# Kernel optimization log

Hardware: AMD Instinct MI355X
Metric: run time of the kernel (lower is better)

Reference implementation:

```python
import jax, jax.numpy as jnp
import numpy as np

TEMP = 0.07
POS_WINDOW = 2
EPS = 1e-8
NEG = -1e9  # finite large-negative for masking (safe under vjp)


def _l2norm(x):
    # matches F.normalize(dim=-1) with eps=1e-12
    n = jnp.sqrt(jnp.sum(x * x, axis=-1, keepdims=True))
    return x / jnp.maximum(n, 1e-12)


def setup_inputs() -> dict:
    key = jax.random.key(0)
    k1, k2, k3, k4, k5 = jax.random.split(key, 5)
    B, T, D = 32, 1024, 256
    eeg_enc = jax.random.normal(k1, (B, T, D), dtype=jnp.float32)
    eye_enc = jax.random.normal(k2, (B, T, D), dtype=jnp.float32)
    mask = jax.random.randint(k3, (B, T), 0, 2, dtype=jnp.int32)
    W_eeg = jax.random.normal(k4, (D, D), dtype=jnp.float32) / np.sqrt(D)
    W_eye = jax.random.normal(k5, (D, D), dtype=jnp.float32) / np.sqrt(D)
    return {"eeg_enc": eeg_enc, "eye_enc": eye_enc, "mask": mask,
            "W_eeg": W_eeg, "W_eye": W_eye}


def reference(eeg_enc, eye_enc, mask, W_eeg, W_eye):
    B, T, D = eeg_enc.shape
    valid = mask > 0  # (B,T)
    # nn.Linear(bias=False): x @ W.T, then L2-normalize
    e = _l2norm(jnp.einsum('btd,ed->bte', eeg_enc, W_eeg))
    v = _l2norm(jnp.einsum('btd,ed->bte', eye_enc, W_eye))
    sims = jnp.einsum('bid,bjd->bij', e, v) / TEMP  # (B,T,T)
    # rank of each valid step within the compressed (gathered) ordering
    rank = jnp.cumsum(valid.astype(jnp.int32), axis=-1) - 1  # (B,T)
    band = jnp.abs(rank[:, :, None] - rank[:, None, :]) <= POS_WINDOW
    pair = valid[:, :, None] & valid[:, None, :]  # both steps valid
    pos = pair & band
    # per-row max over positive (banded) entries
    pos_scores = jnp.max(jnp.where(pos, sims, NEG), axis=-1)  # (B,T)
    # logsumexp over valid columns (the gathered sims row)
    lse = jax.nn.logsumexp(jnp.where(valid[:, None, :], sims, NEG), axis=-1)
    row_loss = -(pos_scores - lse)  # (B,T)
    Tv = jnp.sum(valid, axis=-1)  # (B,)
    per_b = jnp.sum(jnp.where(valid, row_loss, 0.0), axis=-1) / jnp.maximum(Tv, 1)
    per_b = jnp.where(Tv >= 2, per_b, 0.0)  # skip samples with <2 valid steps
    return jnp.sum(per_b) / (B + EPS)
```

## Files before the change

kernel.cpp:

```cpp
#include <hip/hip_runtime.h>
#include <hip/hip_bf16.h>

typedef __attribute__((ext_vector_type(8))) short bf16x8;
typedef __attribute__((ext_vector_type(4))) float f32x4;

#define INVT (1.0f/0.07f)

static __device__ __forceinline__ short f2bf(float f){
    unsigned int u = __float_as_uint(f);
    unsigned int r = (u + 0x7fffu + ((u >> 16) & 1u)) >> 16;
    return (short)r;
}
static __device__ __forceinline__ float bf2f(short s){
    return __uint_as_float(((unsigned int)(unsigned short)s) << 16);
}

static __device__ __forceinline__ void gld16(const void* g, void* l){
    __builtin_amdgcn_global_load_lds(
        (const __attribute__((address_space(1))) unsigned int*)g,
        (__attribute__((address_space(3))) unsigned int*)l, 16, 0, 0);
}

__global__ __launch_bounds__(256) void prep_kernel(const float* __restrict__ Weeg,
                                                   const float* __restrict__ Weye,
                                                   const int* __restrict__ mask,
                                                   short* __restrict__ Wout,
                                                   int* __restrict__ rank,
                                                   int* __restrict__ idx,
                                                   int* __restrict__ Tv,
                                                   float* __restrict__ cb,
                                                   float* __restrict__ bsum){
    __shared__ int ssum[256];
    int tid = threadIdx.x;
    if (blockIdx.x < 512){
        int i = blockIdx.x * 256 + tid;
        float v = (i < 65536) ? Weeg[i] : Weye[i - 65536];
        Wout[i] = f2bf(v);
        return;
    }
    int b = blockIdx.x - 512;
    if (tid == 0) bsum[b] = 0.f;
    int local[4]; int s = 0;
    #pragma unroll
    for (int q = 0; q < 4; ++q){
        int t = tid*4 + q;
        local[q] = (mask[b*1024 + t] > 0) ? 1 : 0;
        s += local[q];
    }
    ssum[tid] = s;
    __syncthreads();
    for (int off = 1; off < 256; off <<= 1){
        int add = (tid >= off) ? ssum[tid - off] : 0;
        __syncthreads();
        ssum[tid] += add;
        __syncthreads();
    }
    int run = ssum[tid] - s;
    #pragma unroll
    for (int q = 0; q < 4; ++q){
        int t = tid*4 + q;
        int g = b*1024 + t;
        run += local[q];
        rank[g] = run - 1;
        cb[g]   = local[q] ? 0.0f : -1e9f;
        if (local[q]) idx[b*1024 + run - 1] = t;
    }
    if (tid == 255) Tv[b] = ssum[255];
}

__global__ __launch_bounds__(256, 2) void proj_kernel(const float* __restrict__ Aeeg,
                                                      const float* __restrict__ Aeye,
                                                      const short* __restrict__ Wbf,
                                                      short* __restrict__ Eout,
                                                      short* __restrict__ Vout){
    __shared__ short sW[2][64 * 256];
    int sel = blockIdx.y;
    const float* A   = sel ? Aeye : Aeeg;
    const short* W   = Wbf + sel * 65536;
    short*       Out = sel ? Vout : Eout;

    int tid = threadIdx.x;
    int w = tid >> 6, lane = tid & 63;
    int l15 = lane & 15, lq = lane >> 4;
    int kb  = lq * 8;
    int row0 = blockIdx.x * 64;

    int ro   = lane >> 5;
    int cs   = lane & 31;
    int s7   = l15 & 7;

    #pragma unroll
    for (int p = 0; p < 8; ++p){
        int rr = (p*2 + ro) & 7;
        gld16(W + (size_t)(w*16 + p*2 + ro)*256 + (cs ^ rr)*8,
              &sW[0][(w*16 + p*2) * 256]);
    }
    #pragma unroll
    for (int p = 0; p < 8; ++p){
        int rr = (p*2 + ro) & 7;
        gld16(W + (size_t)(64 + w*16 + p*2 + ro)*256 + (cs ^ rr)*8,
              &sW[1][(w*16 + p*2) * 256]);
    }

    bf16x8 xf[8];
    {
        const float* ap = A + (size_t)(row0 + w*16 + l15) * 256 + kb;
        #pragma unroll
        for (int g = 0; g < 8; ++g){
            float4 x0 = *(const float4*)(ap + g*32);
            float4 x1 = *(const float4*)(ap + g*32 + 4);
            bf16x8 t;
            t[0]=f2bf(x0.x); t[1]=f2bf(x0.y); t[2]=f2bf(x0.z); t[3]=f2bf(x0.w);
            t[4]=f2bf(x1.x); t[5]=f2bf(x1.y); t[6]=f2bf(x1.z); t[7]=f2bf(x1.w);
            xf[g] = t;
        }
    }

    f32x4 acc[16];
    #pragma unroll
    for (int q = 0; q < 16; ++q) acc[q] = (f32x4){0.f,0.f,0.f,0.f};

    __syncthreads();

    #pragma unroll
    for (int nt = 0; nt < 4; ++nt){
        f32x4 c = acc[nt];
        int rbase = (nt*16 + l15) * 256;
        #pragma unroll
        for (int g = 0; g < 8; ++g){
            bf16x8 wf = *(const bf16x8*)&sW[0][rbase + (((g*4 + lq) ^ s7) << 3)];
            c = __builtin_amdgcn_mfma_f32_16x16x32_bf16(wf, xf[g], c, 0, 0, 0);
        }
        acc[nt] = c;
    }

    __syncthreads();

    #pragma unroll
    for (int p = 0; p < 8; ++p){
        int rr = (p*2 + ro) & 7;
        gld16(W + (size_t)(128 + w*16 + p*2 + ro)*256 + (cs ^ rr)*8,
              &sW[0][(w*16 + p*2) * 256]);
    }
    #pragma unroll
    for (int nt = 0; nt < 4; ++nt){
        f32x4 c = acc[4 + nt];
        int rbase = (nt*16 + l15) * 256;
        #pragma unroll
        for (int g = 0; g < 8; ++g){
            bf16x8 wf = *(const bf16x8*)&sW[1][rbase + (((g*4 + lq) ^ s7) << 3)];
            c = __builtin_amdgcn_mfma_f32_16x16x32_bf16(wf, xf[g], c, 0, 0, 0);
        }
        acc[4 + nt] = c;
    }

    __syncthreads();

    #pragma unroll
    for (int p = 0; p < 8; ++p){
        int rr = (p*2 + ro) & 7;
        gld16(W + (size_t)(192 + w*16 + p*2 + ro)*256 + (cs ^ rr)*8,
              &sW[1][(w*16 + p*2) * 256]);
    }
    #pragma unroll
    for (int nt = 0; nt < 4; ++nt){
        f32x4 c = acc[8 + nt];
        int rbase = (nt*16 + l15) * 256;
        #pragma unroll
        for (int g = 0; g < 8; ++g){
            bf16x8 wf = *(const bf16x8*)&sW[0][rbase + (((g*4 + lq) ^ s7) << 3)];
            c = __builtin_amdgcn_mfma_f32_16x16x32_bf16(wf, xf[g], c, 0, 0, 0);
        }
        acc[8 + nt] = c;
    }

    __syncthreads();

    #pragma unroll
    for (int nt = 0; nt < 4; ++nt){
        f32x4 c = acc[12 + nt];
        int rbase = (nt*16 + l15) * 256;
        #pragma unroll
        for (int g = 0; g < 8; ++g){
            bf16x8 wf = *(const bf16x8*)&sW[1][rbase + (((g*4 + lq) ^ s7) << 3)];
            c = __builtin_amdgcn_mfma_f32_16x16x32_bf16(wf, xf[g], c, 0, 0, 0);
        }
        acc[12 + nt] = c;
    }

    float ss = 0.f;
    #pragma unroll
    for (int q = 0; q < 16; ++q){
        #pragma unroll
        for (int r = 0; r < 4; ++r){ float x = acc[q][r]; ss += x*x; }
    }
    ss += __shfl_xor(ss, 16);
    ss += __shfl_xor(ss, 32);
    float scale = 1.0f / fmaxf(sqrtf(ss), 1e-12f);

    short* twrow = &sW[0][(w*16 + l15) * 256];
    #pragma unroll
    for (int q = 0; q < 16; ++q){
        short4 pk;
        pk.x = f2bf(acc[q][0] * scale);
        pk.y = f2bf(acc[q][1] * scale);
        pk.z = f2bf(acc[q][2] * scale);
        pk.w = f2bf(acc[q][3] * scale);
        int c    = (q >> 2) * 64 + (q & 3) * 16 + lq*4;
        int blk  = (c >> 3) ^ s7;
        *(short4*)(twrow + blk*8 + (c & 7)) = pk;
    }
    short* op = Out + (size_t)(row0 + w*16) * 256;
    #pragma unroll
    for (int p = 0; p < 8; ++p){
        int rloc = p*2 + (lane >> 5);
        int gblk = lane & 31;
        const short* tr = &sW[0][(w*16 + rloc) * 256 + ((gblk ^ (rloc & 7)) * 8)];
        *(int4*)(op + rloc*256 + gblk*8) = *(const int4*)tr;
    }
}

__global__ __launch_bounds__(64) void loss_kernel(const short* __restrict__ E,
                                                  const short* __restrict__ V,
                                                  const float* __restrict__ cb,
                                                  float* __restrict__ psum){
    int n  = blockIdx.x;
    int b  = (((n >> 3) & 3) << 3) | (n & 7);
    int r2 = n >> 5;
    int it = r2 & 15;
    int jq = r2 >> 4;

    int lane = threadIdx.x;
    int l15 = lane & 15, lq = lane >> 4;

    bf16x8 af[4][8];
    {
        const short* ep = E + ((size_t)b*1024 + it*64 + l15) * 256 + lq*8;
        #pragma unroll
        for (int s = 0; s < 4; ++s)
            #pragma unroll
            for (int g = 0; g < 8; ++g)
                af[s][g] = *(const bf16x8*)(ep + s*16*256 + g*32);
    }

    const short* vp  = V  + ((size_t)b*1024 + jq*256 + l15) * 256 + lq*8;
    const float* cbp = cb + b*1024 + jq*256 + l15;

    float ls[4][4];
    #pragma unroll
    for (int s = 0; s < 4; ++s)
        #pragma unroll
        for (int r = 0; r < 4; ++r) ls[s][r] = 0.f;

    bf16x8 ba[8], bb[8];
    #pragma unroll
    for (int g = 0; g < 8; ++g) ba[g] = *(const bf16x8*)(vp + g*32);
    float ca = cbp[0];
    float cbv;

    #pragma unroll 1
    for (int t = 0; t < 8; ++t){
        {
            const short* v1 = vp + (size_t)(2*t + 1) * 16 * 256;
            #pragma unroll
            for (int g = 0; g < 8; ++g) bb[g] = *(const bf16x8*)(v1 + g*32);
            cbv = cbp[(2*t + 1) * 16];
        }
        {
            f32x4 a0 = (f32x4){0.f,0.f,0.f,0.f};
            f32x4 a1 = (f32x4){0.f,0.f,0.f,0.f};
            f32x4 a2 = (f32x4){0.f,0.f,0.f,0.f};
            f32x4 a3 = (f32x4){0.f,0.f,0.f,0.f};
            #pragma unroll
            for (int g = 0; g < 8; ++g){
                a0 = __builtin_amdgcn_mfma_f32_16x16x32_bf16(af[0][g], ba[g], a0, 0, 0, 0);
                a1 = __builtin_amdgcn_mfma_f32_16x16x32_bf16(af[1][g], ba[g], a1, 0, 0, 0);
                a2 = __builtin_amdgcn_mfma_f32_16x16x32_bf16(af[2][g], ba[g], a2, 0, 0, 0);
                a3 = __builtin_amdgcn_mfma_f32_16x16x32_bf16(af[3][g], ba[g], a3, 0, 0, 0);
            }
            #pragma unroll
            for (int r = 0; r < 4; ++r){
                ls[0][r] += __expf(fmaf(a0[r], INVT, ca));
                ls[1][r] += __expf(fmaf(a1[r], INVT, ca));
                ls[2][r] += __expf(fmaf(a2[r], INVT, ca));
                ls[3][r] += __expf(fmaf(a3[r], INVT, ca));
            }
        }
        if (t < 7){
            const short* v2 = vp + (size_t)(2*t + 2) * 16 * 256;
            #pragma unroll
            for (int g = 0; g < 8; ++g) ba[g] = *(const bf16x8*)(v2 + g*32);
            ca = cbp[(2*t + 2) * 16];
        }
        {
            f32x4 a0 = (f32x4){0.f,0.f,0.f,0.f};
            f32x4 a1 = (f32x4){0.f,0.f,0.f,0.f};
            f32x4 a2 = (f32x4){0.f,0.f,0.f,0.f};
            f32x4 a3 = (f32x4){0.f,0.f,0.f,0.f};
            #pragma unroll
            for (int g = 0; g < 8; ++g){
                a0 = __builtin_amdgcn_mfma_f32_16x16x32_bf16(af[0][g], bb[g], a0, 0, 0, 0);
                a1 = __builtin_amdgcn_mfma_f32_16x16x32_bf16(af[1][g], bb[g], a1, 0, 0, 0);
                a2 = __builtin_amdgcn_mfma_f32_16x16x32_bf16(af[2][g], bb[g], a2, 0, 0, 0);
                a3 = __builtin_amdgcn_mfma_f32_16x16x32_bf16(af[3][g], bb[g], a3, 0, 0, 0);
            }
            #pragma unroll
            for (int r = 0; r < 4; ++r){
                ls[0][r] += __expf(fmaf(a0[r], INVT, cbv));
                ls[1][r] += __expf(fmaf(a1[r], INVT, cbv));
                ls[2][r] += __expf(fmaf(a2[r], INVT, cbv));
                ls[3][r] += __expf(fmaf(a3[r], INVT, cbv));
            }
        }
    }

    #pragma unroll
    for (int s = 0; s < 4; ++s)
        #pragma unroll
        for (int r = 0; r < 4; ++r){
            float v = ls[s][r];
            #pragma unroll
            for (int mm = 1; mm < 16; mm <<= 1)
                v += __shfl_xor(v, mm);
            ls[s][r] = v;
        }

    if (l15 == 0){
        float* pp = psum + (size_t)jq*32768 + (size_t)b*1024 + it*64;
        #pragma unroll
        for (int s = 0; s < 4; ++s)
            #pragma unroll
            for (int r = 0; r < 4; ++r)
                pp[s*16 + lq*4 + r] = ls[s][r];
    }
}

__global__ __launch_bounds__(256) void pos_kernel(const short* __restrict__ E,
                                                  const short* __restrict__ V,
                                                  const int* __restrict__ mask,
                                                  const int* __restrict__ rank,
                                                  const int* __restrict__ idx,
                                                  const int* __restrict__ Tv,
                                                  float* __restrict__ pmax){
    int tid = threadIdx.x;
    int gl  = tid & 15;
    int rf  = (blockIdx.x * 256 + tid) >> 4;
    int b   = rf >> 10;
    if (mask[rf] <= 0) return;

    int ri = rank[rf];
    int tv = Tv[b];
    int lo = ri - 2; if (lo < 0) lo = 0;
    int hi = ri + 2; if (hi > tv - 1) hi = tv - 1;

    const short* epp = E + (size_t)rf * 256 + gl * 16;
    float ev[16];
    {
        bf16x8 e0 = *(const bf16x8*)epp;
        bf16x8 e1 = *(const bf16x8*)(epp + 8);
        #pragma unroll
        for (int k = 0; k < 8; ++k){ ev[k] = bf2f(e0[k]); ev[8+k] = bf2f(e1[k]); }
    }
    float pm = -1e30f;
    for (int r = lo; r <= hi; ++r){
        int j = idx[b*1024 + r];
        const short* vpp = V + ((size_t)(b*1024) + j) * 256 + gl * 16;
        bf16x8 v0 = *(const bf16x8*)vpp;
        bf16x8 v1 = *(const bf16x8*)(vpp + 8);
        float s = 0.f;
        #pragma unroll
        for (int k = 0; k < 8; ++k){
            s = fmaf(ev[k],   bf2f(v0[k]), s);
            s = fmaf(ev[8+k], bf2f(v1[k]), s);
        }
        s += __shfl_xor(s, 1);
        s += __shfl_xor(s, 2);
        s += __shfl_xor(s, 4);
        s += __shfl_xor(s, 8);
        pm = fmaxf(pm, s);
    }
    if (gl == 0) pmax[rf] = pm * INVT;
}

__global__ __launch_bounds__(256) void reduce_kernel(const float* __restrict__ psum,
                                                     const float* __restrict__ pmax,
                                                     const int* __restrict__ mask,
                                                     float* __restrict__ bsum){
    int b  = blockIdx.x >> 2;
    int i  = (blockIdx.x & 3) * 256 + threadIdx.x;
    int g  = b*1024 + i;
    float a = 0.f;
    if (mask[g] > 0){
        float ps = psum[g] + psum[g + 32768] + psum[g + 65536] + psum[g + 98304];
        a = logf(ps) - pmax[g];
    }
    #pragma unroll
    for (int m = 1; m < 64; m <<= 1) a += __shfl_xor(a, m);
    if ((threadIdx.x & 63) == 0 && a != 0.f) atomicAdd(&bsum[b], a);
}

__global__ void final_kernel(const float* __restrict__ bsum,
                             const int* __restrict__ Tv,
                             float* __restrict__ out){
    int tid = threadIdx.x;
    float v = 0.f;
    if (tid < 32){
        int tv = Tv[tid];
        if (tv >= 2) v = bsum[tid] / (float)tv;
    }
    #pragma unroll
    for (int m = 1; m < 64; m <<= 1) v += __shfl_xor(v, m);
    if (tid == 0) out[0] = v / 32.0f;
}

extern "C" void kernel_launch(void* const* d_in, const int* in_sizes, int n_in,
                              void* d_out, int out_size, void* d_ws, size_t ws_size,
                              hipStream_t stream) {
    const float* eeg  = (const float*)d_in[0];
    const float* eye  = (const float*)d_in[1];
    const int*   mask = (const int*)d_in[2];
    const float* Weeg = (const float*)d_in[3];
    const float* Weye = (const float*)d_in[4];
    float* out = (float*)d_out;

    char* ws = (char*)d_ws;
    short* e_bf  = (short*)(ws);
    short* v_bf  = (short*)(ws + 16777216);
    short* wbf   = (short*)(ws + 33554432);
    int*   rank  = (int*)  (ws + 33816576);
    int*   idx   = (int*)  (ws + 33947648);
    float* cb    = (float*)(ws + 34078720);
    float* psum  = (float*)(ws + 34209792);
    float* pmax  = (float*)(ws + 34734080);
    int*   Tv    = (int*)  (ws + 34865152);
    float* bsum  = (float*)(ws + 34865280);

    prep_kernel<<<544, 256, 0, stream>>>(Weeg, Weye, mask, wbf, rank, idx, Tv, cb, bsum);
    proj_kernel<<<dim3(512, 2), 256, 0, stream>>>(eeg, eye, wbf, e_bf, v_bf);
    loss_kernel<<<2048, 64, 0, stream>>>(e_bf, v_bf, cb, psum);
    pos_kernel<<<2048, 256, 0, stream>>>(e_bf, v_bf, mask, rank, idx, Tv, pmax);
    reduce_kernel<<<128, 256, 0, stream>>>(psum, pmax, mask, bsum);
    final_kernel<<<1, 64, 0, stream>>>(bsum, Tv, out);
}
```

Baseline: 172.6 us.

## Share V tiles across four waves via double-buffered LDS in loss kernel

Reworks the loss kernel from 64-thread blocks that each load their own V rows from global memory into 256-thread blocks. In these blocks four waves share 16-row V tiles, staged into a swizzled, double-buffered LDS buffer with async global-to-LDS loads. This cuts redundant global/L2 traffic for V by four times and frees the B-operand registers. It adds block-wide barriers each half-iteration and LDS read traffic, and reduces the grid from 2048 to 512 blocks, which may lower latency hiding.

```diff
diff --git a/kernel.cpp b/kernel.cpp
--- a/kernel.cpp
+++ b/kernel.cpp
@@ -220,22 +220,39 @@
     }
 }
 
-__global__ __launch_bounds__(64) void loss_kernel(const short* __restrict__ E,
-                                                  const short* __restrict__ V,
-                                                  const float* __restrict__ cb,
-                                                  float* __restrict__ psum){
-    int n  = blockIdx.x;
-    int b  = (((n >> 3) & 3) << 3) | (n & 7);
-    int r2 = n >> 5;
-    int it = r2 & 15;
-    int jq = r2 >> 4;
-
-    int lane = threadIdx.x;
-    int l15 = lane & 15, lq = lane >> 4;
+__global__ __launch_bounds__(256, 2) void loss_kernel(const short* __restrict__ E,
+                                                      const short* __restrict__ V,
+                                                      const float* __restrict__ cb,
+                                                      float* __restrict__ psum){
+    __shared__ short sV[2][16 * 256];
+
+    int n   = blockIdx.x;
+    int b   = (((n >> 3) & 3) << 3) | (n & 7);
+    int itg = (n >> 5) & 3;
+    int jq  = n >> 7;
+
+    int tid  = threadIdx.x;
+    int w    = tid >> 6, lane = tid & 63;
+    int l15  = lane & 15, lq = lane >> 4;
+    int s7   = l15 & 7;
+    int ro   = lane >> 5;
+    int cs   = lane & 31;
+    int j0   = jq * 256;
+    int i0   = itg * 256 + w * 64;
+
+    const short* Vb = V + (size_t)b * 1024 * 256;
+
+    #pragma unroll
+    for (int c0 = 0; c0 < 2; ++c0){
+        int p  = w*2 + c0;
+        int rr = (p*2 + ro) & 7;
+        gld16(Vb + (size_t)(j0 + p*2 + ro)*256 + (cs ^ rr)*8,
+              &sV[0][(p*2) * 256]);
+    }
 
     bf16x8 af[4][8];
     {
-        const short* ep = E + ((size_t)b*1024 + it*64 + l15) * 256 + lq*8;
+        const short* ep = E + ((size_t)b*1024 + i0 + l15) * 256 + lq*8;
         #pragma unroll
         for (int s = 0; s < 4; ++s)
             #pragma unroll
@@ -243,8 +260,7 @@
                 af[s][g] = *(const bf16x8*)(ep + s*16*256 + g*32);
     }
 
-    const short* vp  = V  + ((size_t)b*1024 + jq*256 + l15) * 256 + lq*8;
-    const float* cbp = cb + b*1024 + jq*256 + l15;
+    const float* cbp = cb + b*1024 + j0 + l15;
 
     float ls[4][4];
     #pragma unroll
@@ -252,31 +268,30 @@
         #pragma unroll
         for (int r = 0; r < 4; ++r) ls[s][r] = 0.f;
 
-    bf16x8 ba[8], bb[8];
-    #pragma unroll
-    for (int g = 0; g < 8; ++g) ba[g] = *(const bf16x8*)(vp + g*32);
-    float ca = cbp[0];
-    float cbv;
+    __syncthreads();
 
     #pragma unroll 1
-    for (int t = 0; t < 8; ++t){
+    for (int tp = 0; tp < 8; ++tp){
+        #pragma unroll
+        for (int c0 = 0; c0 < 2; ++c0){
+            int p  = w*2 + c0;
+            int rr = (p*2 + ro) & 7;
+            gld16(Vb + (size_t)(j0 + (2*tp+1)*16 + p*2 + ro)*256 + (cs ^ rr)*8,
+                  &sV[1][(p*2) * 256]);
+        }
         {
-            const short* v1 = vp + (size_t)(2*t + 1) * 16 * 256;
-            #pragma unroll
-            for (int g = 0; g < 8; ++g) bb[g] = *(const bf16x8*)(v1 + g*32);
-            cbv = cbp[(2*t + 1) * 16];
-        }
-        {
+            float ca = cbp[2*tp*16];
             f32x4 a0 = (f32x4){0.f,0.f,0.f,0.f};
             f32x4 a1 = (f32x4){0.f,0.f,0.f,0.f};
             f32x4 a2 = (f32x4){0.f,0.f,0.f,0.f};
             f32x4 a3 = (f32x4){0.f,0.f,0.f,0.f};
             #pragma unroll
             for (int g = 0; g < 8; ++g){
-                a0 = __builtin_amdgcn_mfma_f32_16x16x32_bf16(af[0][g], ba[g], a0, 0, 0, 0);
-                a1 = __builtin_amdgcn_mfma_f32_16x16x32_bf16(af[1][g], ba[g], a1, 0, 0, 0);
-                a2 = __builtin_amdgcn_mfma_f32_16x16x32_bf16(af[2][g], ba[g], a2, 0, 0, 0);
-                a3 = __builtin_amdgcn_mfma_f32_16x16x32_bf16(af[3][g], ba[g], a3, 0, 0, 0);
+                bf16x8 bf = *(const bf16x8*)&sV[0][l15*256 + (((g*4 + lq) ^ s7) << 3)];
+                a0 = __builtin_amdgcn_mfma_f32_16x16x32_bf16(af[0][g], bf, a0, 0, 0, 0);
+                a1 = __builtin_amdgcn_mfma_f32_16x16x32_bf16(af[1][g], bf, a1, 0, 0, 0);
+                a2 = __builtin_amdgcn_mfma_f32_16x16x32_bf16(af[2][g], bf, a2, 0, 0, 0);
+                a3 = __builtin_amdgcn_mfma_f32_16x16x32_bf16(af[3][g], bf, a3, 0, 0, 0);
             }
             #pragma unroll
             for (int r = 0; r < 4; ++r){
@@ -286,32 +301,40 @@
                 ls[3][r] += __expf(fmaf(a3[r], INVT, ca));
             }
         }
-        if (t < 7){
-            const short* v2 = vp + (size_t)(2*t + 2) * 16 * 256;
-            #pragma unroll
-            for (int g = 0; g < 8; ++g) ba[g] = *(const bf16x8*)(v2 + g*32);
-            ca = cbp[(2*t + 2) * 16];
+        __syncthreads();
+
+        if (tp < 7){
+            #pragma unroll
+            for (int c0 = 0; c0 < 2; ++c0){
+                int p  = w*2 + c0;
+                int rr = (p*2 + ro) & 7;
+                gld16(Vb + (size_t)(j0 + (2*tp+2)*16 + p*2 + ro)*256 + (cs ^ rr)*8,
+                      &sV[0][(p*2) * 256]);
+            }
         }
         {
+            float ca = cbp[(2*tp+1)*16];
             f32x4 a0 = (f32x4){0.f,0.f,0.f,0.f};
             f32x4 a1 = (f32x4){0.f,0.f,0.f,0.f};
             f32x4 a2 = (f32x4){0.f,0.f,0.f,0.f};
             f32x4 a3 = (f32x4){0.f,0.f,0.f,0.f};
             #pragma unroll
             for (int g = 0; g < 8; ++g){
-                a0 = __builtin_amdgcn_mfma_f32_16x16x32_bf16(af[0][g], bb[g], a0, 0, 0, 0);
-                a1 = __builtin_amdgcn_mfma_f32_16x16x32_bf16(af[1][g], bb[g], a1, 0, 0, 0);
-                a2 = __builtin_amdgcn_mfma_f32_16x16x32_bf16(af[2][g], bb[g], a2, 0, 0, 0);
-                a3 = __builtin_amdgcn_mfma_f32_16x16x32_bf16(af[3][g], bb[g], a3, 0, 0, 0);
+                bf16x8 bf = *(const bf16x8*)&sV[1][l15*256 + (((g*4 + lq) ^ s7) << 3)];
+                a0 = __builtin_amdgcn_mfma_f32_16x16x32_bf16(af[0][g], bf, a0, 0, 0, 0);
+                a1 = __builtin_amdgcn_mfma_f32_16x16x32_bf16(af[1][g], bf, a1, 0, 0, 0);
+                a2 = __builtin_amdgcn_mfma_f32_16x16x32_bf16(af[2][g], bf, a2, 0, 0, 0);
+                a3 = __builtin_amdgcn_mfma_f32_16x16x32_bf16(af[3][g], bf, a3, 0, 0, 0);
             }
             #pragma unroll
             for (int r = 0; r < 4; ++r){
-                ls[0][r] += __expf(fmaf(a0[r], INVT, cbv));
-                ls[1][r] += __expf(fmaf(a1[r], INVT, cbv));
-                ls[2][r] += __expf(fmaf(a2[r], INVT, cbv));
-                ls[3][r] += __expf(fmaf(a3[r], INVT, cbv));
+                ls[0][r] += __expf(fmaf(a0[r], INVT, ca));
+                ls[1][r] += __expf(fmaf(a1[r], INVT, ca));
+                ls[2][r] += __expf(fmaf(a2[r], INVT, ca));
+                ls[3][r] += __expf(fmaf(a3[r], INVT, ca));
             }
         }
+        __syncthreads();
     }
 
     #pragma unroll
@@ -326,7 +349,7 @@
         }
 
     if (l15 == 0){
-        float* pp = psum + (size_t)jq*32768 + (size_t)b*1024 + it*64;
+        float* pp = psum + (size_t)jq*32768 + (size_t)b*1024 + i0;
         #pragma unroll
         for (int s = 0; s < 4; ++s)
             #pragma unroll
@@ -437,7 +460,7 @@
 
     prep_kernel<<<544, 256, 0, stream>>>(Weeg, Weye, mask, wbf, rank, idx, Tv, cb, bsum);
     proj_kernel<<<dim3(512, 2), 256, 0, stream>>>(eeg, eye, wbf, e_bf, v_bf);
-    loss_kernel<<<2048, 64, 0, stream>>>(e_bf, v_bf, cb, psum);
+    loss_kernel<<<512, 256, 0, stream>>>(e_bf, v_bf, cb, psum);
     pos_kernel<<<2048, 256, 0, stream>>>(e_bf, v_bf, mask, rank, idx, Tv, pmax);
     reduce_kernel<<<128, 256, 0, stream>>>(psum, pmax, mask, bsum);
     final_kernel<<<1, 64, 0, stream>>>(bsum, Tv, out);
```

New measurement: 159.4 us. 1.08x faster.
